# Kernel optimization log

Measured on AMD Instinct MI355X. Metric: run time of the kernel, lower is better.

Reference implementation:

```python
import jax, jax.numpy as jnp
import numpy as np

N = 100000   # nodes
E = 3200000  # edges
D = 256      # node_dim
H = 64       # hidden (conv1 out)
L = 64       # latent_dim
G = 128      # graphs in batch


def _gcn_conv(x, src, dst, W, b):
    """PyG GCNConv with edge_weight=1: add self-loops, sym deg-norm, scatter-add."""
    n = x.shape[0]
    loop = jnp.arange(n)
    s = jnp.concatenate([src, loop])
    d = jnp.concatenate([dst, loop])
    w = jnp.ones(s.shape[0], x.dtype)
    deg = jax.ops.segment_sum(w, d, num_segments=n)
    dinv = jnp.where(deg > 0, jax.lax.rsqrt(deg), 0.0)
    norm = dinv[s] * w * dinv[d]                      # [E+N]
    h = x @ W                                         # lin (no bias)
    out = jax.ops.segment_sum(h[s] * norm[:, None], d, num_segments=n)
    return out + b


def _mean_pool(z, batch, num_graphs):
    zsum = jax.ops.segment_sum(z, batch, num_segments=num_graphs)
    cnt = jax.ops.segment_sum(jnp.ones(z.shape[0], z.dtype), batch, num_segments=num_graphs)
    return zsum / jnp.clip(cnt, 1.0)[:, None]


def setup_inputs() -> dict:
    key = jax.random.key(0)
    ks = jax.random.split(key, 8)
    x = jax.random.normal(ks[0], (N, D), jnp.float32)
    edge_index = jax.random.randint(ks[1], (2, E), 0, N, dtype=jnp.int64)
    batch = jnp.sort(jax.random.randint(ks[2], (N,), 0, G, dtype=jnp.int64))
    glorot = lambda k, fi, fo: jax.random.normal(k, (fi, fo), jnp.float32) / np.sqrt(fi).astype(np.float32)
    return {
        "x": x, "edge_index": edge_index, "batch": batch,
        "W1": glorot(ks[3], D, H), "b1": jnp.zeros((H,), jnp.float32),
        "W2": glorot(ks[4], H, L), "b2": jnp.zeros((L,), jnp.float32),
        "Wd1": glorot(ks[5], L, 64), "bd1": jnp.zeros((64,), jnp.float32),
        "Wd2": glorot(ks[6], 64, D), "bd2": jnp.zeros((D,), jnp.float32),
    }


def reference(x, edge_index, batch, W1, b1, W2, b2, Wd1, bd1, Wd2, bd2):
    src, dst = edge_index[0], edge_index[1]
    h = jax.nn.relu(_gcn_conv(x, src, dst, W1, b1))
    z = _gcn_conv(h, src, dst, W2, b2)
    z_pool = _mean_pool(z, batch, G)                  # [G, L]
    x_hat = jax.nn.relu(z_pool @ Wd1 + bd1) @ Wd2 + bd2  # [G, D]
    return (x_hat, z_pool)
```

## Files before the change

kernel.cpp:

```cpp
#include <hip/hip_runtime.h>
#include <hip/hip_bf16.h>
#include <hip/hip_fp16.h>
#include <hip/hip_fp8.h>

namespace {
constexpr int kN = 100000;
constexpr int kE = 3200000;
constexpr int kD = 256;
constexpr int kH = 64;
constexpr int kG = 128;

constexpr int kNB   = 782;
constexpr int kCapS = 4608;
constexpr int kCap  = 64;
constexpr int kNPad = 100352;

constexpr size_t kAlign = 512;
constexpr size_t align_up(size_t v) { return (v + kAlign - 1) & ~(kAlign - 1); }

constexpr size_t OFF_CURD = 0;
constexpr size_t OFF_GCNT = OFF_CURD + align_up(kNB * 4);
constexpr size_t OFF_QRAW = OFF_GCNT + kAlign;
constexpr size_t ZERO_BYTES = OFF_QRAW + align_up((size_t)kG * kH * 4);
constexpr size_t OFF_CNT  = ZERO_BYTES;
constexpr size_t OFF_DINV = OFF_CNT + align_up((size_t)kNPad * 4);
constexpr size_t OFF_SD   = OFF_DINV + align_up((size_t)kNPad * 4);
constexpr size_t OFF_REC  = OFF_SD + align_up((size_t)kNB * kCapS * 4);
constexpr size_t OFF_HL   = OFF_REC + align_up((size_t)kNPad * kCap * 4);
constexpr size_t OFF_H2   = OFF_HL + align_up((size_t)(kN + 1) * kH);
}

__device__ __forceinline__ unsigned pack4_fp8(float a, float b, float c, float d) {
#if __has_builtin(__builtin_amdgcn_cvt_pk_fp8_f32)
    int r = 0;
    r = __builtin_amdgcn_cvt_pk_fp8_f32(a, b, r, false);
    r = __builtin_amdgcn_cvt_pk_fp8_f32(c, d, r, true);
    return (unsigned)r;
#else
    __hip_fp8_e4m3 qa(a), qb(b), qc(c), qd(d);
    return (unsigned)qa.__x | ((unsigned)qb.__x << 8)
         | ((unsigned)qc.__x << 16) | ((unsigned)qd.__x << 24);
#endif
}

__device__ __forceinline__ void add8q(float (&acc)[8], uint2 u) {
#if __has_builtin(__builtin_amdgcn_cvt_pk_f32_fp8)
    typedef float v2f __attribute__((ext_vector_type(2)));
    v2f f0 = __builtin_amdgcn_cvt_pk_f32_fp8((int)u.x, false);
    v2f f1 = __builtin_amdgcn_cvt_pk_f32_fp8((int)u.x, true);
    v2f f2 = __builtin_amdgcn_cvt_pk_f32_fp8((int)u.y, false);
    v2f f3 = __builtin_amdgcn_cvt_pk_f32_fp8((int)u.y, true);
    acc[0] += f0.x; acc[1] += f0.y; acc[2] += f1.x; acc[3] += f1.y;
    acc[4] += f2.x; acc[5] += f2.y; acc[6] += f3.x; acc[7] += f3.y;
#else
    #pragma unroll
    for (int j = 0; j < 4; ++j) {
        __hip_fp8_e4m3 v; v.__x = (__hip_fp8_storage_t)((u.x >> (8 * j)) & 0xFF);
        acc[j] += (float)v;
    }
    #pragma unroll
    for (int j = 0; j < 4; ++j) {
        __hip_fp8_e4m3 v; v.__x = (__hip_fp8_storage_t)((u.y >> (8 * j)) & 0xFF);
        acc[4 + j] += (float)v;
    }
#endif
}

__global__ __launch_bounds__(1024) void k_bucket(const int* __restrict__ src,
                                                 const int* __restrict__ dst,
                                                 int* __restrict__ curD,
                                                 unsigned* __restrict__ streamD) {
    __shared__ int cD[kNB], bD[kNB];
    int t = threadIdx.x;
    for (int i = t; i < kNB; i += 1024) cD[i] = 0;
    __syncthreads();
    int e0 = blockIdx.x * 16384;
    #pragma unroll
    for (int k = 0; k < 16; ++k) {
        int e = e0 + k * 1024 + t;
        if (e < kE) atomicAdd(&cD[dst[e] >> 7], 1);
    }
    __syncthreads();
    for (int i = t; i < kNB; i += 1024)
        bD[i] = cD[i] ? atomicAdd(&curD[i], cD[i]) : 0;
    __syncthreads();
    for (int i = t; i < kNB; i += 1024) cD[i] = 0;
    __syncthreads();
    #pragma unroll
    for (int k = 0; k < 16; ++k) {
        int e = e0 + k * 1024 + t;
        if (e < kE) {
            int s = src[e], d = dst[e];
            int pd = bD[d >> 7] + atomicAdd(&cD[d >> 7], 1);
            if (pd < kCapS)
                streamD[(size_t)(d >> 7) * kCapS + pd] =
                    ((unsigned)(d & 127) << 17) | (unsigned)s;
        }
    }
}

__global__ __launch_bounds__(256) void k_fillB(const int* __restrict__ curD,
                                               const unsigned* __restrict__ streamD,
                                               int* __restrict__ rec,
                                               int* __restrict__ cnt) {
    __shared__ int lc[128];
    int b = blockIdx.x, t = threadIdx.x;
    if (t < 128) lc[t] = 0;
    __syncthreads();
    int n = min(curD[b], kCapS);
    const unsigned* sp = streamD + (size_t)b * kCapS;
    for (int i = t; i < n; i += 256) {
        unsigned u = sp[i];
        int dlo = (u >> 17) & 127;
        int slot = atomicAdd(&lc[dlo], 1);
        if (slot < kCap)
            rec[((((size_t)b << 7) | dlo) << 6) + slot] = (int)(u & 0x1FFFF);
    }
    __syncthreads();
    if (t < 128) {
        int d = (b << 7) + t;
        if (d < kNPad) cnt[d] = lc[t];
    }
}

__global__ void k_gcnt(const int* __restrict__ batch, int* __restrict__ gcnt) {
    __shared__ int h[kG];
    int t = threadIdx.x;
    if (t < kG) h[t] = 0;
    __syncthreads();
    for (int i = blockIdx.x * blockDim.x + t; i < kN; i += gridDim.x * blockDim.x)
        atomicAdd(&h[batch[i]], 1);
    __syncthreads();
    if (t < kG && h[t]) atomicAdd(&gcnt[t], h[t]);
}

__global__ void k_dinv(const int* __restrict__ cnt, float* __restrict__ dinv,
                       unsigned* __restrict__ hl8, unsigned* __restrict__ h8) {
    int i = blockIdx.x * blockDim.x + threadIdx.x;
    if (i < kN) dinv[i] = rsqrtf((float)(cnt[i] + 1));
    if (blockIdx.x == 0 && threadIdx.x < 32) {
        int t = threadIdx.x;
        unsigned* p = (t < 16) ? hl8 : h8;
        p[((size_t)kN * kH) / 4 + (t & 15)] = 0u;
    }
}

__global__ __launch_bounds__(256) void k_gemm1(const float* __restrict__ x,
                                               const float* __restrict__ W1,
                                               const float* __restrict__ dinv,
                                               unsigned char* __restrict__ hl8) {
    constexpr int TM = 64;
    constexpr int KC = 32;
    __shared__ float xs[TM][36];
    __shared__ float ws[KC][kH];
    int t = threadIdx.x;
    int tx = t & 15;
    int ty = t >> 4;
    int nb = blockIdx.x * TM;
    float acc[4][4] = {};
    for (int k0 = 0; k0 < kD; k0 += KC) {
        #pragma unroll
        for (int j = 0; j < 2; ++j) {
            int id = t * 2 + j;
            int row = id >> 3;
            int c4 = (id & 7) * 4;
            int node = nb + row;
            if (node >= kN) node = kN - 1;
            float4 v = *(const float4*)(x + (size_t)node * kD + k0 + c4);
            *(float4*)&xs[row][c4] = v;
        }
        #pragma unroll
        for (int j = 0; j < 2; ++j) {
            int id = t * 2 + j;
            int row = id >> 4;
            int c4 = (id & 15) * 4;
            float4 v = *(const float4*)(W1 + (size_t)(k0 + row) * kH + c4);
            *(float4*)&ws[row][c4] = v;
        }
        __syncthreads();
        #pragma unroll
        for (int kk = 0; kk < KC; ++kk) {
            float a0 = xs[ty * 4 + 0][kk];
            float a1 = xs[ty * 4 + 1][kk];
            float a2 = xs[ty * 4 + 2][kk];
            float a3 = xs[ty * 4 + 3][kk];
            float4 b = *(const float4*)&ws[kk][tx * 4];
            acc[0][0] = fmaf(a0, b.x, acc[0][0]); acc[0][1] = fmaf(a0, b.y, acc[0][1]);
            acc[0][2] = fmaf(a0, b.z, acc[0][2]); acc[0][3] = fmaf(a0, b.w, acc[0][3]);
            acc[1][0] = fmaf(a1, b.x, acc[1][0]); acc[1][1] = fmaf(a1, b.y, acc[1][1]);
            acc[1][2] = fmaf(a1, b.z, acc[1][2]); acc[1][3] = fmaf(a1, b.w, acc[1][3]);
            acc[2][0] = fmaf(a2, b.x, acc[2][0]); acc[2][1] = fmaf(a2, b.y, acc[2][1]);
            acc[2][2] = fmaf(a2, b.z, acc[2][2]); acc[2][3] = fmaf(a2, b.w, acc[2][3]);
            acc[3][0] = fmaf(a3, b.x, acc[3][0]); acc[3][1] = fmaf(a3, b.y, acc[3][1]);
            acc[3][2] = fmaf(a3, b.z, acc[3][2]); acc[3][3] = fmaf(a3, b.w, acc[3][3]);
        }
        __syncthreads();
    }
    #pragma unroll
    for (int i = 0; i < 4; ++i) {
        int node = nb + ty * 4 + i;
        if (node < kN) {
            float di = dinv[node];
            unsigned p = pack4_fp8(di * acc[i][0], di * acc[i][1],
                                   di * acc[i][2], di * acc[i][3]);
            *(unsigned*)(hl8 + (size_t)node * kH + tx * 4) = p;
        }
    }
}

__global__ __launch_bounds__(256) void k_conv1(const int* __restrict__ rec,
                                               const int* __restrict__ cnt,
                                               const float* __restrict__ dinv,
                                               const unsigned char* __restrict__ hl8,
                                               const float* __restrict__ b1,
                                               unsigned char* __restrict__ h8) {
    int tid = threadIdx.x;
    int lane = tid & 63;
    int node = blockIdx.x * 4 + (tid >> 6);
    if (node >= kN) return;
    int slot = lane >> 3;
    int fl = lane & 7;
    size_t base = (size_t)node << 6;
    int len = min(cnt[node], kCap);
    float acc0[8] = {}, acc1[8] = {};
    for (int c0 = 0; c0 < len; c0 += 16) {
        int e0 = c0 + slot;
        int e1 = c0 + 8 + slot;
        int s0 = (e0 < len) ? rec[base + e0] : kN;
        int s1 = (e1 < len) ? rec[base + e1] : kN;
        uint2 v0 = *(const uint2*)(hl8 + ((size_t)s0 << 6) + fl * 8);
        uint2 v1 = *(const uint2*)(hl8 + ((size_t)s1 << 6) + fl * 8);
        add8q(acc0, v0);
        add8q(acc1, v1);
    }
    #pragma unroll
    for (int j = 0; j < 8; ++j) acc0[j] += acc1[j];
    #pragma unroll
    for (int d = 8; d < 64; d <<= 1) {
        #pragma unroll
        for (int j = 0; j < 8; ++j) acc0[j] += __shfl_xor(acc0[j], d, 64);
    }
    if (slot == 0) {
        uint2 sv = *(const uint2*)(hl8 + ((size_t)node << 6) + fl * 8);
        add8q(acc0, sv);
        float di = dinv[node];
        float4 ba = *(const float4*)(b1 + fl * 8);
        float4 bb = *(const float4*)(b1 + fl * 8 + 4);
        float bz[8] = {ba.x, ba.y, ba.z, ba.w, bb.x, bb.y, bb.z, bb.w};
        float r[8];
        #pragma unroll
        for (int j = 0; j < 8; ++j)
            r[j] = di * fmaxf(fmaf(di, acc0[j], bz[j]), 0.f);
        uint2 o;
        o.x = pack4_fp8(r[0], r[1], r[2], r[3]);
        o.y = pack4_fp8(r[4], r[5], r[6], r[7]);
        *(uint2*)(h8 + ((size_t)node << 6) + fl * 8) = o;
    }
}

__global__ __launch_bounds__(256) void k_pool3(const int* __restrict__ rec,
                                               const int* __restrict__ cnt,
                                               const float* __restrict__ dinv,
                                               const unsigned char* __restrict__ h8,
                                               const int* __restrict__ batch,
                                               float* __restrict__ q_raw) {
    constexpr int CHUNK = 8;
    int tid = threadIdx.x;
    int lane = tid & 63;
    int wid = blockIdx.x * 4 + (tid >> 6);
    int n0 = wid * CHUNK;
    if (n0 >= kN) return;
    int n1 = n0 + CHUNK; if (n1 > kN) n1 = kN;
    int slot = lane >> 3;
    int fl = lane & 7;
    float racc[8] = {};
    int gcur = batch[n0];
    for (int i = n0; i < n1; ++i) {
        int g = batch[i];
        if (g != gcur) {
            #pragma unroll
            for (int d = 8; d < 64; d <<= 1) {
                #pragma unroll
                for (int j = 0; j < 8; ++j) racc[j] += __shfl_xor(racc[j], d, 64);
            }
            if (lane < 8) {
                #pragma unroll
                for (int j = 0; j < 8; ++j)
                    atomicAdd(&q_raw[(gcur << 6) + fl * 8 + j], racc[j]);
            }
            #pragma unroll
            for (int j = 0; j < 8; ++j) racc[j] = 0.f;
            gcur = g;
        }
        size_t base = (size_t)i << 6;
        int len = min(cnt[i], kCap);
        float ns0[8] = {}, ns1[8] = {};
        for (int c0 = 0; c0 < len; c0 += 16) {
            int e0 = c0 + slot;
            int e1 = c0 + 8 + slot;
            int s0 = (e0 < len) ? rec[base + e0] : kN;
            int s1 = (e1 < len) ? rec[base + e1] : kN;
            uint2 v0 = *(const uint2*)(h8 + ((size_t)s0 << 6) + fl * 8);
            uint2 v1 = *(const uint2*)(h8 + ((size_t)s1 << 6) + fl * 8);
            add8q(ns0, v0);
            add8q(ns1, v1);
        }
        if (slot == 0) {
            uint2 sv = *(const uint2*)(h8 + ((size_t)i << 6) + fl * 8);
            add8q(ns0, sv);
        }
        float di = dinv[i];
        #pragma unroll
        for (int j = 0; j < 8; ++j) racc[j] = fmaf(di, ns0[j] + ns1[j], racc[j]);
    }
    #pragma unroll
    for (int d = 8; d < 64; d <<= 1) {
        #pragma unroll
        for (int j = 0; j < 8; ++j) racc[j] += __shfl_xor(racc[j], d, 64);
    }
    if (lane < 8) {
        #pragma unroll
        for (int j = 0; j < 8; ++j)
            atomicAdd(&q_raw[(gcur << 6) + fl * 8 + j], racc[j]);
    }
}

__global__ __launch_bounds__(64) void k_head(const float* __restrict__ q_raw,
                                             const int* __restrict__ gcnt,
                                             const float* __restrict__ W2,
                                             const float* __restrict__ b2,
                                             const float* __restrict__ Wd1,
                                             const float* __restrict__ bd1,
                                             const float* __restrict__ Wd2,
                                             const float* __restrict__ bd2,
                                             float* __restrict__ out) {
    __shared__ float zm[kH], zp[kH], tt[kH];
    int g = blockIdx.x, c = threadIdx.x;
    int cg = gcnt[g];
    float inv = (cg > 0) ? 1.f / (float)cg : 0.f;
    zm[c] = q_raw[(size_t)g * kH + c] * inv;
    __syncthreads();
    float a = b2[c];
    #pragma unroll 8
    for (int k = 0; k < kH; ++k) a = fmaf(zm[k], W2[k * kH + c], a);
    if (cg == 0) a = 0.f;
    out[(size_t)kG * kD + (size_t)g * kH + c] = a;
    zp[c] = a;
    __syncthreads();
    float t = bd1[c];
    #pragma unroll 8
    for (int k = 0; k < kH; ++k) t = fmaf(zp[k], Wd1[k * 64 + c], t);
    tt[c] = fmaxf(t, 0.f);
    __syncthreads();
    #pragma unroll
    for (int j4 = 0; j4 < 4; ++j4) {
        int col = c + j4 * 64;
        float v = bd2[col];
        #pragma unroll 8
        for (int k = 0; k < 64; ++k) v = fmaf(tt[k], Wd2[k * kD + col], v);
        out[(size_t)g * kD + col] = v;
    }
}

extern "C" void kernel_launch(void* const* d_in, const int* in_sizes, int n_in,
                              void* d_out, int out_size, void* d_ws, size_t ws_size,
                              hipStream_t stream) {
    const float* x    = (const float*)d_in[0];
    const int*   ei   = (const int*)d_in[1];
    const int*   src  = ei;
    const int*   dst  = ei + kE;
    const int*   batch= (const int*)d_in[2];
    const float* W1   = (const float*)d_in[3];
    const float* b1   = (const float*)d_in[4];
    const float* W2   = (const float*)d_in[5];
    const float* b2   = (const float*)d_in[6];
    const float* Wd1  = (const float*)d_in[7];
    const float* bd1  = (const float*)d_in[8];
    const float* Wd2  = (const float*)d_in[9];
    const float* bd2  = (const float*)d_in[10];
    float* out = (float*)d_out;

    char* ws = (char*)d_ws;
    int*           curD  = (int*)(ws + OFF_CURD);
    int*           gcnt  = (int*)(ws + OFF_GCNT);
    float*         q_raw = (float*)(ws + OFF_QRAW);
    int*           cnt   = (int*)(ws + OFF_CNT);
    float*         dinv  = (float*)(ws + OFF_DINV);
    unsigned*      sD    = (unsigned*)(ws + OFF_SD);
    int*           rec   = (int*)(ws + OFF_REC);
    unsigned char* hl8   = (unsigned char*)(ws + OFF_HL);
    unsigned char* h8    = (unsigned char*)(ws + OFF_H2);

    hipMemsetAsync(d_ws, 0, ZERO_BYTES, stream);

    const int nBucketBlocks = (kE + 16383) / 16384;

    k_bucket<<<nBucketBlocks, 1024, 0, stream>>>(src, dst, curD, sD);
    k_fillB<<<kNB, 256, 0, stream>>>(curD, sD, rec, cnt);

    k_gcnt<<<128, 256, 0, stream>>>(batch, gcnt);
    k_dinv<<<(kN + 255) / 256, 256, 0, stream>>>(cnt, dinv,
                                                 (unsigned*)hl8, (unsigned*)h8);

    k_gemm1<<<(kN + 63) / 64, 256, 0, stream>>>(x, W1, dinv, hl8);

    k_conv1<<<(kN + 3) / 4, 256, 0, stream>>>(rec, cnt, dinv, hl8, b1, h8);

    const int nPoolWaves = (kN + 7) / 8;
    k_pool3<<<(nPoolWaves + 3) / 4, 256, 0, stream>>>(rec, cnt, dinv, h8, batch, q_raw);

    k_head<<<kG, 64, 0, stream>>>(q_raw, gcnt, W2, b2, Wd1, bd1, Wd2, bd2, out);
}
```

Baseline: 301.6 us.

## Split fp8 node features into two 32-byte feature slices for gather locality

Stores the fp8 hidden features as two separate feature-half arrays (32 bytes per node each) instead of one 64-byte row. The gather kernels conv1 and pool3 now launch twice as many blocks, and each block handles one half, so the working set for random gathers per pass is halved to fit better in cache. In exchange, the edge index lists and degree data are read twice, and there are more blocks and atomics.

```diff
diff --git a/kernel.cpp b/kernel.cpp
--- a/kernel.cpp
+++ b/kernel.cpp
@@ -14,6 +14,8 @@
 constexpr int kCapS = 4608;
 constexpr int kCap  = 64;
 constexpr int kNPad = 100352;
+
+constexpr size_t kSlBytes = (size_t)(kN + 1) * 32;
 
 constexpr size_t kAlign = 512;
 constexpr size_t align_up(size_t v) { return (v + kAlign - 1) & ~(kAlign - 1); }
@@ -27,7 +29,7 @@
 constexpr size_t OFF_SD   = OFF_DINV + align_up((size_t)kNPad * 4);
 constexpr size_t OFF_REC  = OFF_SD + align_up((size_t)kNB * kCapS * 4);
 constexpr size_t OFF_HL   = OFF_REC + align_up((size_t)kNPad * kCap * 4);
-constexpr size_t OFF_H2   = OFF_HL + align_up((size_t)(kN + 1) * kH);
+constexpr size_t OFF_H2   = OFF_HL + align_up(2 * kSlBytes);
 }
 
 __device__ __forceinline__ unsigned pack4_fp8(float a, float b, float c, float d) {
@@ -43,25 +45,17 @@
 #endif
 }
 
-__device__ __forceinline__ void add8q(float (&acc)[8], uint2 u) {
+__device__ __forceinline__ void add4q(float (&acc)[4], unsigned u) {
 #if __has_builtin(__builtin_amdgcn_cvt_pk_f32_fp8)
     typedef float v2f __attribute__((ext_vector_type(2)));
-    v2f f0 = __builtin_amdgcn_cvt_pk_f32_fp8((int)u.x, false);
-    v2f f1 = __builtin_amdgcn_cvt_pk_f32_fp8((int)u.x, true);
-    v2f f2 = __builtin_amdgcn_cvt_pk_f32_fp8((int)u.y, false);
-    v2f f3 = __builtin_amdgcn_cvt_pk_f32_fp8((int)u.y, true);
+    v2f f0 = __builtin_amdgcn_cvt_pk_f32_fp8((int)u, false);
+    v2f f1 = __builtin_amdgcn_cvt_pk_f32_fp8((int)u, true);
     acc[0] += f0.x; acc[1] += f0.y; acc[2] += f1.x; acc[3] += f1.y;
-    acc[4] += f2.x; acc[5] += f2.y; acc[6] += f3.x; acc[7] += f3.y;
 #else
     #pragma unroll
     for (int j = 0; j < 4; ++j) {
-        __hip_fp8_e4m3 v; v.__x = (__hip_fp8_storage_t)((u.x >> (8 * j)) & 0xFF);
+        __hip_fp8_e4m3 v; v.__x = (__hip_fp8_storage_t)((u >> (8 * j)) & 0xFF);
         acc[j] += (float)v;
-    }
-    #pragma unroll
-    for (int j = 0; j < 4; ++j) {
-        __hip_fp8_e4m3 v; v.__x = (__hip_fp8_storage_t)((u.y >> (8 * j)) & 0xFF);
-        acc[4 + j] += (float)v;
     }
 #endif
 }
@@ -141,7 +135,9 @@
     if (blockIdx.x == 0 && threadIdx.x < 32) {
         int t = threadIdx.x;
         unsigned* p = (t < 16) ? hl8 : h8;
-        p[((size_t)kN * kH) / 4 + (t & 15)] = 0u;
+        int s = (t >> 3) & 1;
+        int j = t & 7;
+        p[(s * kSlBytes) / 4 + (size_t)kN * 8 + j] = 0u;
     }
 }
 
@@ -196,6 +192,8 @@
         }
         __syncthreads();
     }
+    int slice = tx >> 3;
+    int off = (tx & 7) * 4;
     #pragma unroll
     for (int i = 0; i < 4; ++i) {
         int node = nb + ty * 4 + i;
@@ -203,7 +201,7 @@
             float di = dinv[node];
             unsigned p = pack4_fp8(di * acc[i][0], di * acc[i][1],
                                    di * acc[i][2], di * acc[i][3]);
-            *(unsigned*)(hl8 + (size_t)node * kH + tx * 4) = p;
+            *(unsigned*)(hl8 + slice * kSlBytes + (size_t)node * 32 + off) = p;
         }
     }
 }
@@ -216,45 +214,43 @@
                                                unsigned char* __restrict__ h8) {
     int tid = threadIdx.x;
     int lane = tid & 63;
-    int node = blockIdx.x * 4 + (tid >> 6);
+    int slice = blockIdx.x & 1;
+    int node = (blockIdx.x >> 1) * 4 + (tid >> 6);
     if (node >= kN) return;
     int slot = lane >> 3;
     int fl = lane & 7;
+    const unsigned char* hsl = hl8 + slice * kSlBytes;
     size_t base = (size_t)node << 6;
     int len = min(cnt[node], kCap);
-    float acc0[8] = {}, acc1[8] = {};
+    float a0[4] = {}, a1[4] = {};
     for (int c0 = 0; c0 < len; c0 += 16) {
         int e0 = c0 + slot;
         int e1 = c0 + 8 + slot;
         int s0 = (e0 < len) ? rec[base + e0] : kN;
         int s1 = (e1 < len) ? rec[base + e1] : kN;
-        uint2 v0 = *(const uint2*)(hl8 + ((size_t)s0 << 6) + fl * 8);
-        uint2 v1 = *(const uint2*)(hl8 + ((size_t)s1 << 6) + fl * 8);
-        add8q(acc0, v0);
-        add8q(acc1, v1);
-    }
-    #pragma unroll
-    for (int j = 0; j < 8; ++j) acc0[j] += acc1[j];
+        unsigned v0 = *(const unsigned*)(hsl + (size_t)s0 * 32 + fl * 4);
+        unsigned v1 = *(const unsigned*)(hsl + (size_t)s1 * 32 + fl * 4);
+        add4q(a0, v0);
+        add4q(a1, v1);
+    }
+    #pragma unroll
+    for (int j = 0; j < 4; ++j) a0[j] += a1[j];
     #pragma unroll
     for (int d = 8; d < 64; d <<= 1) {
         #pragma unroll
-        for (int j = 0; j < 8; ++j) acc0[j] += __shfl_xor(acc0[j], d, 64);
+        for (int j = 0; j < 4; ++j) a0[j] += __shfl_xor(a0[j], d, 64);
     }
     if (slot == 0) {
-        uint2 sv = *(const uint2*)(hl8 + ((size_t)node << 6) + fl * 8);
-        add8q(acc0, sv);
+        unsigned sv = *(const unsigned*)(hsl + (size_t)node * 32 + fl * 4);
+        add4q(a0, sv);
         float di = dinv[node];
-        float4 ba = *(const float4*)(b1 + fl * 8);
-        float4 bb = *(const float4*)(b1 + fl * 8 + 4);
-        float bz[8] = {ba.x, ba.y, ba.z, ba.w, bb.x, bb.y, bb.z, bb.w};
-        float r[8];
-        #pragma unroll
-        for (int j = 0; j < 8; ++j)
-            r[j] = di * fmaxf(fmaf(di, acc0[j], bz[j]), 0.f);
-        uint2 o;
-        o.x = pack4_fp8(r[0], r[1], r[2], r[3]);
-        o.y = pack4_fp8(r[4], r[5], r[6], r[7]);
-        *(uint2*)(h8 + ((size_t)node << 6) + fl * 8) = o;
+        float4 bz = *(const float4*)(b1 + slice * 32 + fl * 4);
+        float r0 = di * fmaxf(fmaf(di, a0[0], bz.x), 0.f);
+        float r1 = di * fmaxf(fmaf(di, a0[1], bz.y), 0.f);
+        float r2 = di * fmaxf(fmaf(di, a0[2], bz.z), 0.f);
+        float r3 = di * fmaxf(fmaf(di, a0[3], bz.w), 0.f);
+        unsigned o = pack4_fp8(r0, r1, r2, r3);
+        *(unsigned*)(h8 + slice * kSlBytes + (size_t)node * 32 + fl * 4) = o;
     }
 }
 
@@ -267,13 +263,15 @@
     constexpr int CHUNK = 8;
     int tid = threadIdx.x;
     int lane = tid & 63;
-    int wid = blockIdx.x * 4 + (tid >> 6);
+    int slice = blockIdx.x & 1;
+    int wid = (blockIdx.x >> 1) * 4 + (tid >> 6);
     int n0 = wid * CHUNK;
     if (n0 >= kN) return;
     int n1 = n0 + CHUNK; if (n1 > kN) n1 = kN;
     int slot = lane >> 3;
     int fl = lane & 7;
-    float racc[8] = {};
+    const unsigned char* hsl = h8 + slice * kSlBytes;
+    float racc[4] = {};
     int gcur = batch[n0];
     for (int i = n0; i < n1; ++i) {
         int g = batch[i];
@@ -281,47 +279,47 @@
             #pragma unroll
             for (int d = 8; d < 64; d <<= 1) {
                 #pragma unroll
-                for (int j = 0; j < 8; ++j) racc[j] += __shfl_xor(racc[j], d, 64);
+                for (int j = 0; j < 4; ++j) racc[j] += __shfl_xor(racc[j], d, 64);
             }
             if (lane < 8) {
                 #pragma unroll
-                for (int j = 0; j < 8; ++j)
-                    atomicAdd(&q_raw[(gcur << 6) + fl * 8 + j], racc[j]);
+                for (int j = 0; j < 4; ++j)
+                    atomicAdd(&q_raw[(gcur << 6) + slice * 32 + fl * 4 + j], racc[j]);
             }
             #pragma unroll
-            for (int j = 0; j < 8; ++j) racc[j] = 0.f;
+            for (int j = 0; j < 4; ++j) racc[j] = 0.f;
             gcur = g;
         }
         size_t base = (size_t)i << 6;
         int len = min(cnt[i], kCap);
-        float ns0[8] = {}, ns1[8] = {};
+        float ns0[4] = {}, ns1[4] = {};
         for (int c0 = 0; c0 < len; c0 += 16) {
             int e0 = c0 + slot;
             int e1 = c0 + 8 + slot;
             int s0 = (e0 < len) ? rec[base + e0] : kN;
             int s1 = (e1 < len) ? rec[base + e1] : kN;
-            uint2 v0 = *(const uint2*)(h8 + ((size_t)s0 << 6) + fl * 8);
-            uint2 v1 = *(const uint2*)(h8 + ((size_t)s1 << 6) + fl * 8);
-            add8q(ns0, v0);
-            add8q(ns1, v1);
+            unsigned v0 = *(const unsigned*)(hsl + (size_t)s0 * 32 + fl * 4);
+            unsigned v1 = *(const unsigned*)(hsl + (size_t)s1 * 32 + fl * 4);
+            add4q(ns0, v0);
+            add4q(ns1, v1);
         }
         if (slot == 0) {
-            uint2 sv = *(const uint2*)(h8 + ((size_t)i << 6) + fl * 8);
-            add8q(ns0, sv);
+            unsigned sv = *(const unsigned*)(hsl + (size_t)i * 32 + fl * 4);
+            add4q(ns0, sv);
         }
         float di = dinv[i];
         #pragma unroll
-        for (int j = 0; j < 8; ++j) racc[j] = fmaf(di, ns0[j] + ns1[j], racc[j]);
+        for (int j = 0; j < 4; ++j) racc[j] = fmaf(di, ns0[j] + ns1[j], racc[j]);
     }
     #pragma unroll
     for (int d = 8; d < 64; d <<= 1) {
         #pragma unroll
-        for (int j = 0; j < 8; ++j) racc[j] += __shfl_xor(racc[j], d, 64);
+        for (int j = 0; j < 4; ++j) racc[j] += __shfl_xor(racc[j], d, 64);
     }
     if (lane < 8) {
         #pragma unroll
-        for (int j = 0; j < 8; ++j)
-            atomicAdd(&q_raw[(gcur << 6) + fl * 8 + j], racc[j]);
+        for (int j = 0; j < 4; ++j)
+            atomicAdd(&q_raw[(gcur << 6) + slice * 32 + fl * 4 + j], racc[j]);
     }
 }
 
@@ -404,10 +402,10 @@
 
     k_gemm1<<<(kN + 63) / 64, 256, 0, stream>>>(x, W1, dinv, hl8);
 
-    k_conv1<<<(kN + 3) / 4, 256, 0, stream>>>(rec, cnt, dinv, hl8, b1, h8);
+    k_conv1<<<((kN + 3) / 4) * 2, 256, 0, stream>>>(rec, cnt, dinv, hl8, b1, h8);
 
     const int nPoolWaves = (kN + 7) / 8;
-    k_pool3<<<(nPoolWaves + 3) / 4, 256, 0, stream>>>(rec, cnt, dinv, h8, batch, q_raw);
+    k_pool3<<<((nPoolWaves + 3) / 4) * 2, 256, 0, stream>>>(rec, cnt, dinv, h8, batch, q_raw);
 
     k_head<<<kG, 64, 0, stream>>>(q_raw, gcnt, W2, b2, Wd1, bd1, Wd2, bd2, out);
 }
```

Result: slower. 319.1 us (+5.8%).
